# Kernel optimization log

Measured on AMD Instinct MI355X. Metric: run time of the kernel, lower is better.

Reference implementation:

```python
import jax, jax.numpy as jnp
import numpy as np

H = 1024          # hidden_size
I = 4096          # intermediate_size
TAU = 9           # hashcode_len
LN_EPS = 1e-12    # layer_norm_eps


def setup_inputs() -> dict:
    key = jax.random.key(0)
    k1, k2, k3, k4 = jax.random.split(key, 4)
    return {
        "hidden_states": jax.random.normal(k1, (4, 2048, H), jnp.float32),
        "ln_weight": jnp.ones((H,), jnp.float32),
        "ln_bias": jnp.zeros((H,), jnp.float32),
        "k_weight": 0.02 * jax.random.normal(k2, (I, H), jnp.float32),
        "q_weight": 0.02 * jax.random.normal(k3, (I, H), jnp.float32),
        "bias": 0.001 * jax.random.normal(k4, (H,), jnp.float32),
    }


def _l2_normalize(x):
    # matches F.normalize(x, dim=-1): x / max(||x||, 1e-12)
    n = jnp.sqrt(jnp.sum(x * x, axis=-1, keepdims=True))
    return x / jnp.maximum(n, 1e-12)


def reference(hidden_states, ln_weight, ln_bias, k_weight, q_weight, bias):
    lead_shape = hidden_states.shape[:-1]
    x = hidden_states.reshape(-1, H)  # [N, H]

    # LayerNorm
    mu = jnp.mean(x, axis=-1, keepdims=True)
    var = jnp.mean(jnp.square(x - mu), axis=-1, keepdims=True)
    x = (x - mu) * jax.lax.rsqrt(var + LN_EPS) * ln_weight + ln_bias

    # YOSO expectation kernel: B_ij = (1 - arccos(<q_i, k_j>)/pi)^tau
    Q = _l2_normalize(x)         # [N, H]
    K = _l2_normalize(k_weight)  # [I, H]
    s = jnp.clip(jnp.einsum('nh,ih->ni', Q, K), -1.0 + 1e-6, 1.0 - 1e-6)
    B = jnp.power(1.0 - jnp.arccos(s) / jnp.pi, TAU)  # [N, I]

    X = jnp.einsum('ni,ih->nh', B, q_weight)  # V = q_weight
    X = _l2_normalize(X) + bias
    return X.reshape(*lead_shape, H)
```

## Files before the change

### kernel.cpp

```cpp
#include <hip/hip_runtime.h>

#define HD 1024
#define ID 4096
#define NR 8192

typedef float f32x4 __attribute__((ext_vector_type(4)));
typedef __bf16 bf16x8 __attribute__((ext_vector_type(8)));
typedef int i32x8 __attribute__((ext_vector_type(8)));

__device__ inline ushort f2bf(float f) {
    union { float f; unsigned u; } v; v.f = f;
    unsigned u = v.u;
    unsigned r = (u + 0x7fffu + ((u >> 16) & 1u)) >> 16;
    return (ushort)r;
}

__device__ inline float wave_sum(float v) {
#pragma unroll
    for (int o = 32; o > 0; o >>= 1) v += __shfl_xor(v, o, 64);
    return v;
}

__device__ __forceinline__ float yoso_act(float v) {
    float s = fminf(fmaxf(v, -0.999999f), 0.999999f);
    float a = fabsf(s);
    float p = 0.49998557f + a * (-0.06751706f + a * (0.02363794f - a * 0.00596170f));
    float q = sqrtf(1.0f - a) * p;
    float tt = (s >= 0.0f) ? 1.0f - q : q;
    float t2 = tt * tt, t4 = t2 * t2, t8 = t4 * t4;
    return t8 * tt;
}

__global__ __launch_bounds__(256, 3) void gemm1f_kernel(
    const unsigned char* __restrict__ Ap, const unsigned char* __restrict__ Bp,
    ushort* __restrict__ Cp, int N, int K) {
    __shared__ unsigned char la[128 * 128] __attribute__((aligned(16)));
    __shared__ unsigned char lb[128 * 128] __attribute__((aligned(16)));
    const int tid = threadIdx.x;
    const int w = tid >> 6, lane = tid & 63;
    const int bid = blockIdx.x;
    const int xcd = bid & 7, cu = (bid >> 3) & 31, rnd = bid >> 8;
    const int brow = (xcd * 8 + (cu >> 2)) * 128;
    const int bcol = (rnd * 4 + (cu & 3)) * 128;
    const int wr = (w >> 1) * 64;
    const int wc = (w & 1) * 64;
    f32x4 acc[4][4] = {};
    const int srow = lane >> 3;
    const int scolb = ((lane & 7) ^ (lane >> 3)) << 4;

    for (int k0 = 0; k0 < K; k0 += 128) {
#pragma unroll
        for (int it = 0; it < 4; ++it) {
            const int rb = w * 32 + it * 8;
            const unsigned char* ga = Ap + (size_t)(brow + rb + srow) * K + k0 + scolb;
            const unsigned char* gb = Bp + (size_t)(bcol + rb + srow) * K + k0 + scolb;
            __builtin_amdgcn_global_load_lds(
                (const __attribute__((address_space(1))) void*)ga,
                (__attribute__((address_space(3))) void*)&la[rb * 128], 16, 0, 0);
            __builtin_amdgcn_global_load_lds(
                (const __attribute__((address_space(1))) void*)gb,
                (__attribute__((address_space(3))) void*)&lb[rb * 128], 16, 0, 0);
        }
        __syncthreads();
        i32x8 af[4], bfr[4];
        const int base = (lane >> 4) << 5;
#pragma unroll
        for (int m = 0; m < 4; ++m) {
            const int row = wr + m * 16 + (lane & 15);
            const int key = (row & 7) << 4;
            const uint4 lo = *(const uint4*)(la + row * 128 + (base ^ key));
            const uint4 hi = *(const uint4*)(la + row * 128 + ((base + 16) ^ key));
            af[m] = (i32x8){(int)lo.x, (int)lo.y, (int)lo.z, (int)lo.w,
                            (int)hi.x, (int)hi.y, (int)hi.z, (int)hi.w};
        }
#pragma unroll
        for (int n = 0; n < 4; ++n) {
            const int row = wc + n * 16 + (lane & 15);
            const int key = (row & 7) << 4;
            const uint4 lo = *(const uint4*)(lb + row * 128 + (base ^ key));
            const uint4 hi = *(const uint4*)(lb + row * 128 + ((base + 16) ^ key));
            bfr[n] = (i32x8){(int)lo.x, (int)lo.y, (int)lo.z, (int)lo.w,
                             (int)hi.x, (int)hi.y, (int)hi.z, (int)hi.w};
        }
#pragma unroll
        for (int m = 0; m < 4; ++m)
#pragma unroll
            for (int n = 0; n < 4; ++n)
                acc[m][n] = __builtin_amdgcn_mfma_scale_f32_16x16x128_f8f6f4(
                    af[m], bfr[n], acc[m][n], 0, 0,
                    0, 0x7F7F7F7F, 0, 0x7F7F7F7F);
        __syncthreads();
    }
    const int crow0 = brow + wr + ((lane >> 4) << 2);
    const int ccol0 = bcol + wc + (lane & 15);
#pragma unroll
    for (int m = 0; m < 4; ++m)
#pragma unroll
        for (int n = 0; n < 4; ++n)
#pragma unroll
            for (int r = 0; r < 4; ++r) {
                int row = crow0 + m * 16 + r;
                int col = ccol0 + n * 16;
                Cp[(size_t)row * N + col] =
                    f2bf(yoso_act(acc[m][n][r] * 0.00390625f));
            }
}

__global__ __launch_bounds__(512) void gemm2d_kernel(
    const ushort* __restrict__ Ap, const ushort* __restrict__ Bp,
    float* __restrict__ Cv, int N, int K, int nt) {
    __shared__ char lds[98304] __attribute__((aligned(16)));
    const int tid = threadIdx.x;
    const int w = tid >> 6, lane = tid & 63;
    const int wm = w >> 1, wn = w & 1;
    const int bid = blockIdx.x;
    const int xcd = bid & 7, cu = bid >> 3;
    const int brow = (xcd * 4 + (cu >> 3)) * 256;
    const int bcol = (cu & 7) * 128;
    const int srow = lane >> 3;
    const int scolb = ((lane & 7) ^ (lane >> 3)) << 4;

    f32x4 acc[4][4] = {};

    auto stage = [&](int t, int db) {
#pragma unroll
        for (int u = 0; u < 4; ++u) {
            int grow = brow + u * 64 + w * 8 + srow;
            const char* src = (const char*)Ap + ((size_t)grow * K + t * 64) * 2 + scolb;
            __builtin_amdgcn_global_load_lds(
                (const __attribute__((address_space(1))) void*)src,
                (__attribute__((address_space(3))) void*)&lds[db * 32768 + u * 8192 + w * 1024],
                16, 0, 0);
        }
#pragma unroll
        for (int u = 0; u < 2; ++u) {
            int grow = bcol + u * 64 + w * 8 + srow;
            const char* src = (const char*)Bp + ((size_t)grow * K + t * 64) * 2 + scolb;
            __builtin_amdgcn_global_load_lds(
                (const __attribute__((address_space(1))) void*)src,
                (__attribute__((address_space(3))) void*)&lds[65536 + db * 16384 + u * 8192 + w * 1024],
                16, 0, 0);
        }
    };

    stage(0, 0);
    asm volatile("s_waitcnt vmcnt(0)" ::: "memory");
    __builtin_amdgcn_s_barrier();

    for (int t = 0; t < nt; ++t) {
        const int db = t & 1;
        const bool more = (t + 1 < nt);
        if (more) stage(t + 1, db ^ 1);
#pragma unroll
        for (int ks = 0; ks < 2; ++ks) {
            bf16x8 af[4], bfr[4];
            const int chunk = ks * 4 + (lane >> 4);
#pragma unroll
            for (int m = 0; m < 4; ++m) {
                int row = wm * 64 + m * 16 + (lane & 15);
                af[m] = *(const bf16x8*)(lds + db * 32768 + row * 128 +
                                         ((chunk ^ (row & 7)) << 4));
            }
#pragma unroll
            for (int n = 0; n < 4; ++n) {
                int row = wn * 64 + n * 16 + (lane & 15);
                bfr[n] = *(const bf16x8*)(lds + 65536 + db * 16384 + row * 128 +
                                          ((chunk ^ (row & 7)) << 4));
            }
#pragma unroll
            for (int m = 0; m < 4; ++m)
#pragma unroll
                for (int n = 0; n < 4; ++n)
                    acc[m][n] = __builtin_amdgcn_mfma_f32_16x16x32_bf16(
                        af[m], bfr[n], acc[m][n], 0, 0, 0);
        }
        if (more) {
            __builtin_amdgcn_sched_barrier(0);
            asm volatile("s_waitcnt vmcnt(0)" ::: "memory");
            __builtin_amdgcn_s_barrier();
        }
    }

    const int crow0 = brow + wm * 64 + ((lane >> 4) << 2);
    const int ccol0 = bcol + wn * 64 + (lane & 15);
#pragma unroll
    for (int m = 0; m < 4; ++m)
#pragma unroll
        for (int n = 0; n < 4; ++n)
#pragma unroll
            for (int r = 0; r < 4; ++r) {
                int row = crow0 + m * 16 + r;
                int col = ccol0 + n * 16;
                Cv[(size_t)row * N + col] = acc[m][n][r];
            }
}

__global__ __launch_bounds__(256) void prep_kernel(
    const float* __restrict__ hs, const float* __restrict__ lnw,
    const float* __restrict__ lnb, const float* __restrict__ kw,
    const float* __restrict__ qw, unsigned char* __restrict__ Qf,
    unsigned char* __restrict__ Kf, ushort* __restrict__ VT) {
    __shared__ float smem[64][65];
    const int b = blockIdx.x, t = threadIdx.x;
    const int lane = t & 63, wid = t >> 6;
    if (b < NR) {
        const float4 v = reinterpret_cast<const float4*>(hs + (size_t)b * HD)[t];
        float s  = v.x + v.y + v.z + v.w;
        float ss = v.x*v.x + v.y*v.y + v.z*v.z + v.w*v.w;
        s = wave_sum(s); ss = wave_sum(ss);
        if (lane == 0) { smem[0][wid] = s; smem[1][wid] = ss; }
        __syncthreads();
        float st  = smem[0][0] + smem[0][1] + smem[0][2] + smem[0][3];
        float sst = smem[1][0] + smem[1][1] + smem[1][2] + smem[1][3];
        float mu   = st * (1.0f / HD);
        float var  = sst * (1.0f / HD) - mu * mu;
        float rstd = rsqrtf(var + 1e-12f);
        const float4 wv = reinterpret_cast<const float4*>(lnw)[t];
        const float4 bv = reinterpret_cast<const float4*>(lnb)[t];
        float y0 = (v.x - mu) * rstd * wv.x + bv.x;
        float y1 = (v.y - mu) * rstd * wv.y + bv.y;
        float y2 = (v.z - mu) * rstd * wv.z + bv.z;
        float y3 = (v.w - mu) * rstd * wv.w + bv.w;
        float n2 = wave_sum(y0*y0 + y1*y1 + y2*y2 + y3*y3);
        if (lane == 0) smem[2][wid] = n2;
        __syncthreads();
        float nt2 = smem[2][0] + smem[2][1] + smem[2][2] + smem[2][3];
        float sc = 16.0f / fmaxf(sqrtf(nt2), 1e-12f);
        int r = __builtin_amdgcn_cvt_pk_fp8_f32(y0 * sc, y1 * sc, 0, false);
        r = __builtin_amdgcn_cvt_pk_fp8_f32(y2 * sc, y3 * sc, r, true);
        reinterpret_cast<int*>(Qf + (size_t)b * HD)[t] = r;
    } else if (b < NR + ID) {
        const int row = b - NR;
        const float4 v = reinterpret_cast<const float4*>(kw + (size_t)row * HD)[t];
        float n2 = wave_sum(v.x*v.x + v.y*v.y + v.z*v.z + v.w*v.w);
        if (lane == 0) smem[0][wid] = n2;
        __syncthreads();
        float nt2 = smem[0][0] + smem[0][1] + smem[0][2] + smem[0][3];
        float sc = 16.0f / fmaxf(sqrtf(nt2), 1e-12f);
        int r = __builtin_amdgcn_cvt_pk_fp8_f32(v.x * sc, v.y * sc, 0, false);
        r = __builtin_amdgcn_cvt_pk_fp8_f32(v.z * sc, v.w * sc, r, true);
        reinterpret_cast<int*>(Kf + (size_t)row * HD)[t] = r;
    } else {
        const int b2 = b - NR - ID;
        const int bi = (b2 & 63) * 64, bh = (b2 >> 6) * 64;
        const int r0 = t >> 4, c0 = (t & 15) << 2;
#pragma unroll
        for (int rr = 0; rr < 64; rr += 16) {
            float4 val = *reinterpret_cast<const float4*>(
                &qw[(size_t)(bi + rr + r0) * HD + bh + c0]);
            smem[rr + r0][c0 + 0] = val.x; smem[rr + r0][c0 + 1] = val.y;
            smem[rr + r0][c0 + 2] = val.z; smem[rr + r0][c0 + 3] = val.w;
        }
        __syncthreads();
#pragma unroll
        for (int rr = 0; rr < 64; rr += 16) {
            ushort4 o;
            o.x = f2bf(smem[c0 + 0][rr + r0]);
            o.y = f2bf(smem[c0 + 1][rr + r0]);
            o.z = f2bf(smem[c0 + 2][rr + r0]);
            o.w = f2bf(smem[c0 + 3][rr + r0]);
            *reinterpret_cast<ushort4*>(&VT[(size_t)(bh + rr + r0) * ID + bi + c0]) = o;
        }
    }
}

__global__ __launch_bounds__(256) void outnorm_kernel(
    float* __restrict__ X, const float* __restrict__ bias) {
    __shared__ float red2[4];
    const int row = blockIdx.x, t = threadIdx.x;
    const int lane = t & 63, wid = t >> 6;
    float4 v = reinterpret_cast<float4*>(X + (size_t)row * HD)[t];
    float n2 = wave_sum(v.x*v.x + v.y*v.y + v.z*v.z + v.w*v.w);
    if (lane == 0) red2[wid] = n2;
    __syncthreads();
    float nt = red2[0] + red2[1] + red2[2] + red2[3];
    float sc = 1.0f / fmaxf(sqrtf(nt), 1e-12f);
    const float4 bv = reinterpret_cast<const float4*>(bias)[t];
    float4 o;
    o.x = v.x * sc + bv.x; o.y = v.y * sc + bv.y;
    o.z = v.z * sc + bv.z; o.w = v.w * sc + bv.w;
    reinterpret_cast<float4*>(X + (size_t)row * HD)[t] = o;
}

extern "C" void kernel_launch(void* const* d_in, const int* in_sizes, int n_in,
                              void* d_out, int out_size, void* d_ws, size_t ws_size,
                              hipStream_t stream) {
    const float* hs   = (const float*)d_in[0];
    const float* lnw  = (const float*)d_in[1];
    const float* lnb  = (const float*)d_in[2];
    const float* kw   = (const float*)d_in[3];
    const float* qw   = (const float*)d_in[4];
    const float* bias = (const float*)d_in[5];
    float* out = (float*)d_out;

    char* ws = (char*)d_ws;
    unsigned char* Qf = (unsigned char*)(ws);
    unsigned char* Kf = (unsigned char*)(ws + (size_t)8388608);
    ushort* VT   = (ushort*)(ws + (size_t)12582912);
    ushort* Bmat = (ushort*)(ws + (size_t)20971520);

    prep_kernel<<<NR + ID + 1024, 256, 0, stream>>>(hs, lnw, lnb, kw, qw, Qf, Kf, VT);
    gemm1f_kernel<<<(NR / 128) * (ID / 128), 256, 0, stream>>>(
        Qf, Kf, Bmat, ID, HD);
    gemm2d_kernel<<<(NR / 256) * (HD / 128), 512, 0, stream>>>(
        Bmat, VT, out, HD, ID, ID / 64);
    outnorm_kernel<<<NR, 256, 0, stream>>>(out, bias);
}
```

Baseline: 154.1 us.

## Triple-buffer LDS in second GEMM with vmcnt-based prefetch two tiles ahead

The second GEMM (B x V) moves from double to triple buffering in LDS (144 KiB) and prefetches tile t+2 while computing tile t. It waits with a partial vmcnt(6) and uses a single barrier per iteration instead of a full drain at the end of each iteration. The aim is to hide global-to-LDS load latency behind MFMA work. The cost is more LDS per block, which keeps occupancy at one 512-thread block per CU.

Result: no change. 153.3 us (-0.5%).

```diff
diff --git a/kernel.cpp b/kernel.cpp
--- a/kernel.cpp
+++ b/kernel.cpp
@@ -106,10 +106,10 @@
             }
 }
 
-__global__ __launch_bounds__(512) void gemm2d_kernel(
+__global__ __launch_bounds__(512) void gemm2t_kernel(
     const ushort* __restrict__ Ap, const ushort* __restrict__ Bp,
     float* __restrict__ Cv, int N, int K, int nt) {
-    __shared__ char lds[98304] __attribute__((aligned(16)));
+    __shared__ char lds[147456] __attribute__((aligned(16)));
     const int tid = threadIdx.x;
     const int w = tid >> 6, lane = tid & 63;
     const int wm = w >> 1, wn = w & 1;
@@ -122,14 +122,14 @@
 
     f32x4 acc[4][4] = {};
 
-    auto stage = [&](int t, int db) {
+    auto stage = [&](int t, int b) {
 #pragma unroll
         for (int u = 0; u < 4; ++u) {
             int grow = brow + u * 64 + w * 8 + srow;
             const char* src = (const char*)Ap + ((size_t)grow * K + t * 64) * 2 + scolb;
             __builtin_amdgcn_global_load_lds(
                 (const __attribute__((address_space(1))) void*)src,
-                (__attribute__((address_space(3))) void*)&lds[db * 32768 + u * 8192 + w * 1024],
+                (__attribute__((address_space(3))) void*)&lds[b * 32768 + u * 8192 + w * 1024],
                 16, 0, 0);
         }
 #pragma unroll
@@ -138,19 +138,26 @@
             const char* src = (const char*)Bp + ((size_t)grow * K + t * 64) * 2 + scolb;
             __builtin_amdgcn_global_load_lds(
                 (const __attribute__((address_space(1))) void*)src,
-                (__attribute__((address_space(3))) void*)&lds[65536 + db * 16384 + u * 8192 + w * 1024],
+                (__attribute__((address_space(3))) void*)&lds[98304 + b * 16384 + u * 8192 + w * 1024],
                 16, 0, 0);
         }
     };
 
     stage(0, 0);
-    asm volatile("s_waitcnt vmcnt(0)" ::: "memory");
-    __builtin_amdgcn_s_barrier();
-
+    stage(1, 1);
+
+    int bt = 0;
     for (int t = 0; t < nt; ++t) {
-        const int db = t & 1;
-        const bool more = (t + 1 < nt);
-        if (more) stage(t + 1, db ^ 1);
+        const bool more2 = (t + 2 < nt);
+        if (t + 1 < nt) asm volatile("s_waitcnt vmcnt(6)" ::: "memory");
+        else            asm volatile("s_waitcnt vmcnt(0)" ::: "memory");
+        __builtin_amdgcn_sched_barrier(0);
+        __builtin_amdgcn_s_barrier();
+        __builtin_amdgcn_sched_barrier(0);
+        if (more2) {
+            int b2 = bt + 2; if (b2 >= 3) b2 -= 3;
+            stage(t + 2, b2);
+        }
 #pragma unroll
         for (int ks = 0; ks < 2; ++ks) {
             bf16x8 af[4], bfr[4];
@@ -158,13 +165,13 @@
 #pragma unroll
             for (int m = 0; m < 4; ++m) {
                 int row = wm * 64 + m * 16 + (lane & 15);
-                af[m] = *(const bf16x8*)(lds + db * 32768 + row * 128 +
+                af[m] = *(const bf16x8*)(lds + bt * 32768 + row * 128 +
                                          ((chunk ^ (row & 7)) << 4));
             }
 #pragma unroll
             for (int n = 0; n < 4; ++n) {
                 int row = wn * 64 + n * 16 + (lane & 15);
-                bfr[n] = *(const bf16x8*)(lds + 65536 + db * 16384 + row * 128 +
+                bfr[n] = *(const bf16x8*)(lds + 98304 + bt * 16384 + row * 128 +
                                           ((chunk ^ (row & 7)) << 4));
             }
 #pragma unroll
@@ -174,11 +181,7 @@
                     acc[m][n] = __builtin_amdgcn_mfma_f32_16x16x32_bf16(
                         af[m], bfr[n], acc[m][n], 0, 0, 0);
         }
-        if (more) {
-            __builtin_amdgcn_sched_barrier(0);
-            asm volatile("s_waitcnt vmcnt(0)" ::: "memory");
-            __builtin_amdgcn_s_barrier();
-        }
+        ++bt; if (bt >= 3) bt -= 3;
     }
 
     const int crow0 = brow + wm * 64 + ((lane >> 4) << 2);
@@ -302,7 +305,7 @@
     prep_kernel<<<NR + ID + 1024, 256, 0, stream>>>(hs, lnw, lnb, kw, qw, Qf, Kf, VT);
     gemm1f_kernel<<<(NR / 128) * (ID / 128), 256, 0, stream>>>(
         Qf, Kf, Bmat, ID, HD);
-    gemm2d_kernel<<<(NR / 256) * (HD / 128), 512, 0, stream>>>(
+    gemm2t_kernel<<<(NR / 256) * (HD / 128), 512, 0, stream>>>(
         Bmat, VT, out, HD, ID, ID / 64);
     outnorm_kernel<<<NR, 256, 0, stream>>>(out, bias);
 }
```
